# Kernel optimization log

Measured on AMD Instinct MI355X. Metric: run time of the kernel, lower is better.

## Reference

```python
import jax, jax.numpy as jnp
import numpy as np

B, N, K, D_IN, D, L = 8, 8192, 6, 3, 256, 5
EPS_LN = 1e-5


def layernorm(x, g, b):
    m = jnp.mean(x, axis=-1, keepdims=True)
    v = jnp.mean((x - m) ** 2, axis=-1, keepdims=True)
    return (x - m) * jax.lax.rsqrt(v + EPS_LN) * g + b


def spmm_mean(v, knn):
    # sparse adj matmul: out[j] = sum_{n: j in knn[n]} v[n], then / k
    n, k = knn.shape[-2], knn.shape[-1]
    src = jnp.repeat(jnp.arange(n), k)  # [N*K]

    def one(vb, kb):
        return jnp.zeros_like(vb).at[kb.reshape(-1)].add(vb[src])

    return jax.vmap(one)(v, knn) / (k + 1e-6)


def grf_layer(h, knn, qkv_w, out_w, out_b, hops=3):
    q, k, v = jnp.split(h @ qkv_w, 3, axis=-1)
    for _ in range(hops):
        v = spmm_mean(v, knn)
        k = spmm_mean(k, knn)
    attn = jnp.sum(q * k, axis=-1, keepdims=True)
    return (attn * v) @ out_w + out_b


def linear_attention(h, qkv_w, out_w, out_b):
    q, k, v = jnp.split(h @ qkv_w, 3, axis=-1)
    q = jax.nn.relu(q) + 1e-6
    k = jax.nn.relu(k) + 1e-6
    kv = jnp.einsum('bnd,bne->bde', k, v)
    z = 1.0 / (jnp.einsum('bnd,bd->bn', q, k.sum(axis=1)) + 1e-6)
    attn = jnp.einsum('bnd,bde,bn->bne', q, kv, z)
    return attn @ out_w + out_b


def setup_inputs() -> dict:
    key = jax.random.key(0)
    ks = jax.random.split(key, 12)
    s = 0.02
    return {
        'x': jax.random.normal(ks[0], (B, N, D_IN), jnp.float32),
        'knn': jax.random.randint(ks[1], (B, N, K), 0, N, jnp.int32),
        'emb_w': jax.random.normal(ks[2], (D_IN, D), jnp.float32) * s,
        'emb_b': jnp.zeros((D,), jnp.float32),
        'norm_g': jnp.ones((2 * L, D), jnp.float32),
        'norm_b': jnp.zeros((2 * L, D), jnp.float32),
        'grf_qkv': jax.random.normal(ks[3], (L, D, 3 * D), jnp.float32) * s,
        'grf_outw': jax.random.normal(ks[4], (L, D, D), jnp.float32) * s,
        'grf_outb': jnp.zeros((L, D), jnp.float32),
        'attn_qkv': jax.random.normal(ks[5], (L, D, 3 * D), jnp.float32) * s,
        'attn_outw': jax.random.normal(ks[6], (L, D, D), jnp.float32) * s,
        'attn_outb': jnp.zeros((L, D), jnp.float32),
        'head_w': jax.random.normal(ks[7], (D, 3), jnp.float32) * s,
        'head_b': jnp.zeros((3,), jnp.float32),
    }


def reference(x, knn, emb_w, emb_b, norm_g, norm_b, grf_qkv, grf_outw, grf_outb,
              attn_qkv, attn_outw, attn_outb, head_w, head_b):
    h = x @ emb_w + emb_b
    for i in range(L):
        h = h + grf_layer(layernorm(h, norm_g[2 * i], norm_b[2 * i]), knn,
                          grf_qkv[i], grf_outw[i], grf_outb[i])
        h = h + linear_attention(layernorm(h, norm_g[2 * i + 1], norm_b[2 * i + 1]),
                                 attn_qkv[i], attn_outw[i], attn_outb[i])
    return h @ head_w + head_b
```

## Files before the change

kernel.cpp:

```cpp
#include <hip/hip_runtime.h>

#define BB 8
#define NN 8192
#define KK 6
#define DD 256
#define LL 5
#define NE (BB*NN*KK)
#define PLANE (NN*DD)
#define INV6 (1.0f/6.000001f)

typedef unsigned short u16;
typedef __attribute__((ext_vector_type(8))) _Float16 h8;
typedef __attribute__((ext_vector_type(8))) unsigned short us8;
typedef __attribute__((ext_vector_type(4))) float f32x4;

__device__ __forceinline__ u16 f2h(float f){
  union { _Float16 h; u16 u; } c; c.h = (_Float16)f; return c.u;
}
__device__ __forceinline__ float h2f(u16 u){
  union { _Float16 h; u16 u; } c; c.u = u; return (float)c.h;
}

__device__ __forceinline__ void ldscp(const u16* g, u16* l){
  __builtin_amdgcn_global_load_lds(
      (const __attribute__((address_space(1))) void*)g,
      (__attribute__((address_space(3))) void*)l, 16, 0, 0);
}

__global__ void k_count(const int* __restrict__ knn, int* __restrict__ off){
  int e = blockIdx.x*256 + threadIdx.x;
  if(e >= NE) return;
  int b = e / (NN*KK);
  int j = knn[e];
  atomicAdd(&off[b*(NN+1) + 1 + j], 1);
}

__global__ __launch_bounds__(1024) void k_scan(int* __restrict__ offAll){
  __shared__ int lds[1024];
  __shared__ int carry_s;
  int* off = offAll + blockIdx.x*(NN+1);
  const int len = NN+1;
  int t = threadIdx.x;
  if(t==0) carry_s = 0;
  __syncthreads();
  for(int base=0; base<len; base+=1024){
    int x = (base+t < len) ? off[base+t] : 0;
    lds[t] = x; __syncthreads();
    for(int s=1; s<1024; s<<=1){
      int v = (t>=s) ? lds[t-s] : 0;
      __syncthreads();
      lds[t] += v;
      __syncthreads();
    }
    int incl = lds[t];
    int carry = carry_s;
    __syncthreads();
    if(base+t < len) off[base+t] = incl + carry;
    if(t==1023) carry_s = carry + incl;
    __syncthreads();
  }
}

__global__ void k_fill(const int* __restrict__ knn, int* __restrict__ cursor, int* __restrict__ srcE){
  int e = blockIdx.x*256 + threadIdx.x;
  if(e >= NE) return;
  int b = e / (NN*KK);
  int n = (e % (NN*KK)) / KK;
  int j = knn[e];
  int pos = atomicAdd(&cursor[b*(NN+1) + j], 1);
  srcE[(long)b*NN*KK + pos] = n;
}

__global__ __launch_bounds__(256) void k_prepw(const float* __restrict__ W, u16* __restrict__ Wt, int N){
  int n = blockIdx.x, l = blockIdx.y, k = threadIdx.x;
  float x = W[((long)l*256 + k)*N + n];
  u16 hb = f2h(x);
  Wt[(((long)l*2 + 0)*N + n)*256 + k] = hb;
  Wt[(((long)l*2 + 1)*N + n)*256 + k] = f2h(x - h2f(hb));
}

__global__ __launch_bounds__(256) void k_embed(const float* __restrict__ x, const float* __restrict__ ew,
                        const float* __restrict__ eb, float* __restrict__ h){
  int g = blockIdx.x, z = blockIdx.y, d = threadIdx.x;
  const float* xp = x + ((long)z*NN + g)*3;
  h[(long)z*PLANE + (long)g*DD + d] = xp[0]*ew[0*DD+d] + xp[1]*ew[1*DD+d] + xp[2]*ew[2*DD+d] + eb[d];
}

__global__ __launch_bounds__(256) void k_ln(const float* __restrict__ h, const float* __restrict__ g,
                     const float* __restrict__ bia, u16* __restrict__ out){
  long z = blockIdx.y;
  int row = blockIdx.x*4 + (threadIdx.x >> 6);
  int lane = threadIdx.x & 63;
  const float4 x = *(const float4*)(h + z*PLANE + (long)row*DD + lane*4);
  float s  = x.x + x.y + x.z + x.w;
  float s2 = x.x*x.x + x.y*x.y + x.z*x.z + x.w*x.w;
  for(int o=1;o<64;o<<=1){ s += __shfl_xor(s,o); s2 += __shfl_xor(s2,o); }
  float m = s*(1.0f/256.0f);
  float var = s2*(1.0f/256.0f) - m*m;
  float r = rsqrtf(var + 1e-5f);
  const float4 gu = *(const float4*)(g + lane*4);
  const float4 bu = *(const float4*)(bia + lane*4);
  ushort4 o4;
  o4.x = f2h((x.x-m)*r*gu.x + bu.x);
  o4.y = f2h((x.y-m)*r*gu.y + bu.y);
  o4.z = f2h((x.z-m)*r*gu.z + bu.z);
  o4.w = f2h((x.w-m)*r*gu.w + bu.w);
  *(ushort4*)(out + z*PLANE + (long)row*DD + lane*4) = o4;
}

template<int BM,int BN,bool ASPLIT,bool BF32,bool BSPLIT>
__global__ __launch_bounds__(256) void k_mgemm(
    const u16* __restrict__ A, long aStride, long aLoOff, int K, int kSplit,
    const void* __restrict__ Bv, long bStride, long bLoOff,
    const float* __restrict__ rowscale, long rsStride,
    const float* __restrict__ bias,
    u16* __restrict__ o0, u16* __restrict__ o1, u16* __restrict__ o2,
    long oStride, int reluMask, long oLoOff,
    float* __restrict__ accOut, long hStride)
{
  constexpr int WM = BM/2, WN = BN/2, MT = WM/16, NT = WN/16;
  constexpr int STG = BM*32*(ASPLIT?2:1) + BN*32*(BSPLIT?2:1);
  constexpr int EPI = (BM==128) ? 32*132*2 : 0;
  constexpr int SM  = (STG > EPI) ? STG : EPI;
  __shared__ __align__(16) u16 smem[SM];
  u16* Ahi = smem;
  u16* Alo = smem + BM*32;
  u16* Bhi = smem + BM*32*(ASPLIT?2:1);
  u16* Blo = Bhi + BN*32;
  float* epi = (float*)smem;

  const int t = threadIdx.x;
  const int nz = blockIdx.z;
  const long z = nz / kSplit;
  const int chunk = nz % kSplit;
  const int kLen = K / kSplit, kLo = chunk * kLen;
  const int rowTile = blockIdx.x*BM, colTile = blockIdx.y*BN;
  const int l = t & 63, w = t >> 6;
  const int wr = w >> 1, wc = w & 1;
  const int lm = l & 15, kq = l >> 4;

  f32x4 acc[MT][NT];
  #pragma unroll
  for(int mt=0;mt<MT;mt++)
    #pragma unroll
    for(int nt=0;nt<NT;nt++) acc[mt][nt] = (f32x4){0.f,0.f,0.f,0.f};

  for(int k0=kLo; k0<kLo+kLen; k0+=32){
    __syncthreads();
    {
      constexpr int NCH = BM/64;
      #pragma unroll
      for(int li=0; li<NCH; li++){
        int f = li*256 + t;
        int row = f>>2, c = (f&3)*8;
        const u16* gp = A + z*aStride + (long)(rowTile+row)*K + k0 + c;
        ldscp(gp, &Ahi[f*8]);
        if constexpr (ASPLIT) ldscp(gp + aLoOff, &Alo[f*8]);
      }
    }
    if constexpr (BF32){
      constexpr int NCH = BN/64;
      #pragma unroll
      for(int li=0; li<NCH; li++){
        int f = li*256 + t;
        int row = f>>2, c = (f&3)*8;
        const float* src = (const float*)Bv + z*bStride + (long)(colTile+row)*K + k0 + c;
        float4 v0 = ((const float4*)src)[0], v1 = ((const float4*)src)[1];
        us8 hv;
        hv[0]=f2h(v0.x); hv[1]=f2h(v0.y); hv[2]=f2h(v0.z); hv[3]=f2h(v0.w);
        hv[4]=f2h(v1.x); hv[5]=f2h(v1.y); hv[6]=f2h(v1.z); hv[7]=f2h(v1.w);
        *(us8*)&Bhi[f*8] = hv;
      }
    } else {
      constexpr int NCH = BN/64;
      #pragma unroll
      for(int li=0; li<NCH; li++){
        int f = li*256 + t;
        int row = f>>2, c = (f&3)*8;
        const u16* gp = (const u16*)Bv + z*bStride + (long)(colTile+row)*K + k0 + c;
        ldscp(gp, &Bhi[f*8]);
        if constexpr (BSPLIT) ldscp(gp + bLoOff, &Blo[f*8]);
      }
    }
    __syncthreads();
    h8 ah[MT], al[MT], bh[NT], bl[NT];
    #pragma unroll
    for(int mt=0;mt<MT;mt++){
      int idx = (wr*WM + mt*16 + lm)*32 + kq*8;
      ah[mt] = *(const h8*)&Ahi[idx];
      if constexpr (ASPLIT) al[mt] = *(const h8*)&Alo[idx];
    }
    #pragma unroll
    for(int nt=0;nt<NT;nt++){
      int idx = (wc*WN + nt*16 + lm)*32 + kq*8;
      bh[nt] = *(const h8*)&Bhi[idx];
      if constexpr (BSPLIT) bl[nt] = *(const h8*)&Blo[idx];
    }
    #pragma unroll
    for(int mt=0;mt<MT;mt++)
      #pragma unroll
      for(int nt=0;nt<NT;nt++){
        acc[mt][nt] = __builtin_amdgcn_mfma_f32_16x16x32_f16(ah[mt], bh[nt], acc[mt][nt], 0, 0, 0);
        if constexpr (BSPLIT)
          acc[mt][nt] = __builtin_amdgcn_mfma_f32_16x16x32_f16(ah[mt], bl[nt], acc[mt][nt], 0, 0, 0);
        if constexpr (ASPLIT)
          acc[mt][nt] = __builtin_amdgcn_mfma_f32_16x16x32_f16(al[mt], bh[nt], acc[mt][nt], 0, 0, 0);
      }
  }

  if constexpr (BM == 128){
    const int sec = colTile >> 8;
    u16* osec = (sec==0) ? o0 : ((sec==1) ? o1 : o2);
    const bool relu = (reluMask >> sec) & 1;
    #pragma unroll
    for(int mt=0;mt<MT;mt++){
      __syncthreads();
      #pragma unroll
      for(int r=0;r<4;r++){
        int gm = rowTile + wr*64 + mt*16 + kq*4 + r;
        float sc = rowscale ? rowscale[z*rsStride + gm] : 1.0f;
        int rl = wr*16 + kq*4 + r;
        #pragma unroll
        for(int nt=0;nt<NT;nt++)
          epi[rl*132 + wc*64 + nt*16 + lm] = acc[mt][nt][r]*sc;
      }
      __syncthreads();
      #pragma unroll
      for(int ss=0;ss<2;ss++){
        int s = ss*256 + t;
        int rl = s >> 4, sc8 = (s & 15)*8;
        int gm2 = rowTile + (rl>>4)*64 + mt*16 + (rl & 15);
        float v[8];
        #pragma unroll
        for(int j=0;j<8;j++) v[j] = epi[rl*132 + sc8 + j];
        if(bias){
          const float* bp = bias + colTile + sc8;
          #pragma unroll
          for(int j=0;j<8;j++) v[j] += bp[j];
        }
        if(accOut){
          float* hp = accOut + z*hStride + (long)gm2*256 + colTile + sc8;
          float4 h0 = ((float4*)hp)[0], h1 = ((float4*)hp)[1];
          h0.x += v[0]; h0.y += v[1]; h0.z += v[2]; h0.w += v[3];
          h1.x += v[4]; h1.y += v[5]; h1.z += v[6]; h1.w += v[7];
          ((float4*)hp)[0] = h0; ((float4*)hp)[1] = h1;
        } else {
          us8 o8;
          #pragma unroll
          for(int j=0;j<8;j++){
            float vv = v[j];
            if(relu) vv = fmaxf(vv, 0.f) + 1e-6f;
            o8[j] = f2h(vv);
          }
          *(us8*)(osec + z*oStride + (long)gm2*256 + ((colTile + sc8) & 255)) = o8;
        }
      }
    }
  } else {
    #pragma unroll
    for(int mt=0;mt<MT;mt++){
      #pragma unroll
      for(int r=0;r<4;r++){
        int gm = rowTile + wr*WM + mt*16 + kq*4 + r;
        float sc = rowscale ? rowscale[z*rsStride + gm] : 1.0f;
        if(accOut){
          float* hp = accOut + z*hStride + (long)gm*256;
          if(kSplit > 1){
            #pragma unroll
            for(int nt=0;nt<NT;nt++){
              int gc = colTile + wc*WN + nt*16 + lm;
              atomicAdd(&hp[gc], acc[mt][nt][r]);
            }
          } else {
            #pragma unroll
            for(int nt=0;nt<NT;nt++){
              int gc = colTile + wc*WN + nt*16 + lm;
              hp[gc] += acc[mt][nt][r]*sc + (bias ? bias[gc] : 0.f);
            }
          }
        } else {
          #pragma unroll
          for(int nt=0;nt<NT;nt++){
            int gc = colTile + wc*WN + nt*16 + lm;
            int sec = gc >> 8;
            u16* o = (sec==0) ? o0 : ((sec==1) ? o1 : o2);
            float val = acc[mt][nt][r]*sc + (bias ? bias[gc] : 0.f);
            if((reluMask >> sec) & 1) val = fmaxf(val, 0.f) + 1e-6f;
            if(sec==0 && oLoOff){
              u16* oo = o0 + 2*z*oStride + (long)gm*256 + (gc & 255);
              u16 hb = f2h(val);
              oo[0] = hb;
              oo[oLoOff] = f2h(val - h2f(hb));
            } else {
              o[z*oStride + (long)gm*256 + (gc & 255)] = f2h(val);
            }
          }
        }
      }
    }
  }
}

__global__ __launch_bounds__(256) void k_fusedout(
    const u16* __restrict__ A, const u16* __restrict__ B, long bStride, long bLoOff,
    const float* __restrict__ rowscale, const float* __restrict__ bias,
    float* __restrict__ h,
    const float* __restrict__ lnG, const float* __restrict__ lnB,
    u16* __restrict__ Lout)
{
  constexpr int SMU = 64*32 + 2*256*32;
  __shared__ __align__(16) u16 smem[SMU];
  u16* As = smem;
  u16* Bh = smem + 64*32;
  u16* Bl = Bh + 256*32;
  float* epi = (float*)smem;

  const int t = threadIdx.x;
  const long z = blockIdx.z;
  const int rowTile = blockIdx.x*64;
  const int l = t & 63, w = t >> 6;
  const int wr = w >> 1, wc = w & 1;
  const int lm = l & 15, kq = l >> 4;
  const u16* Ab = A + z*PLANE;
  const u16* Bb = B + z*bStride;

  f32x4 acc[2][8];
  #pragma unroll
  for(int mt=0;mt<2;mt++)
    #pragma unroll
    for(int nt=0;nt<8;nt++) acc[mt][nt] = (f32x4){0.f,0.f,0.f,0.f};

  for(int k0=0; k0<256; k0+=32){
    __syncthreads();
    {
      ldscp(Ab + (long)(rowTile+(t>>2))*256 + k0 + (t&3)*8, &As[t*8]);
    }
    #pragma unroll
    for(int li=0; li<4; li++){
      int f = li*256 + t;
      int row = f>>2, c = (f&3)*8;
      const u16* gp = Bb + (long)row*256 + k0 + c;
      ldscp(gp, &Bh[f*8]);
      ldscp(gp + bLoOff, &Bl[f*8]);
    }
    __syncthreads();
    h8 af[2], bh[8], bl[8];
    #pragma unroll
    for(int mt=0;mt<2;mt++)
      af[mt] = *(const h8*)&As[(wr*32 + mt*16 + lm)*32 + kq*8];
    #pragma unroll
    for(int nt=0;nt<8;nt++){
      int idx = (wc*128 + nt*16 + lm)*32 + kq*8;
      bh[nt] = *(const h8*)&Bh[idx];
      bl[nt] = *(const h8*)&Bl[idx];
    }
    #pragma unroll
    for(int mt=0;mt<2;mt++)
      #pragma unroll
      for(int nt=0;nt<8;nt++){
        acc[mt][nt] = __builtin_amdgcn_mfma_f32_16x16x32_f16(af[mt], bh[nt], acc[mt][nt], 0, 0, 0);
        acc[mt][nt] = __builtin_amdgcn_mfma_f32_16x16x32_f16(af[mt], bl[nt], acc[mt][nt], 0, 0, 0);
      }
  }

  #pragma unroll
  for(int mt=0;mt<2;mt++){
    __syncthreads();
    #pragma unroll
    for(int r=0;r<4;r++){
      int rl = wr*16 + kq*4 + r;
      int gm = rowTile + wr*32 + mt*16 + kq*4 + r;
      float sc = rowscale ? rowscale[z*NN + gm] : 1.0f;
      #pragma unroll
      for(int nt=0;nt<8;nt++)
        epi[rl*260 + wc*128 + nt*16 + lm] = acc[mt][nt][r]*sc;
    }
    __syncthreads();
    #pragma unroll
    for(int ss=0;ss<8;ss++){
      int s = ss*256 + t;
      int rl = s >> 6;
      int c4 = (s & 63)*4;
      int gm = rowTile + (rl>>4)*32 + mt*16 + (rl & 15);
      float4 e = *(float4*)&epi[rl*260 + c4];
      float4 x;
      x.x = e.x + bias[c4+0];
      x.y = e.y + bias[c4+1];
      x.z = e.z + bias[c4+2];
      x.w = e.w + bias[c4+3];
      float* hp = h + z*PLANE + (long)gm*256 + c4;
      float4 h0 = *(float4*)hp;
      x.x += h0.x; x.y += h0.y; x.z += h0.z; x.w += h0.w;
      *(float4*)hp = x;
      if(lnG){
        float sA = x.x + x.y + x.z + x.w;
        float s2 = x.x*x.x + x.y*x.y + x.z*x.z + x.w*x.w;
        for(int o=1;o<64;o<<=1){ sA += __shfl_xor(sA,o); s2 += __shfl_xor(s2,o); }
        float m = sA*(1.0f/256.0f);
        float var = s2*(1.0f/256.0f) - m*m;
        float rr = rsqrtf(var + 1e-5f);
        const float4 gu = *(const float4*)(lnG + c4);
        const float4 bu = *(const float4*)(lnB + c4);
        ushort4 o4;
        o4.x = f2h((x.x-m)*rr*gu.x + bu.x);
        o4.y = f2h((x.y-m)*rr*gu.y + bu.y);
        o4.z = f2h((x.z-m)*rr*gu.z + bu.z);
        o4.w = f2h((x.w-m)*rr*gu.w + bu.w);
        *(ushort4*)(Lout + z*PLANE + (long)gm*256 + c4) = o4;
      }
    }
  }
}

template<int MODE>
__global__ __launch_bounds__(256) void k_spmm2(
    const u16* __restrict__ kin, const u16* __restrict__ vin,
    const int* __restrict__ offB, const int* __restrict__ srcB,
    u16* __restrict__ kout, u16* __restrict__ vout,
    const u16* __restrict__ q, float* __restrict__ rs){
  long z = blockIdx.x;
  const int* off = offB + z*(NN+1);
  const int* sE  = srcB + z*(long)NN*KK;

  if constexpr (MODE == 0){
    const u16* kp = kin + z*PLANE;
    const u16* vp = vin + z*PLANE;
    int row = blockIdx.y*16 + (threadIdx.x >> 4);
    int d8 = blockIdx.z*128 + (threadIdx.x & 15)*8;
    int s0 = off[row], s1 = off[row+1];
    float ak[8], av[8];
    #pragma unroll
    for(int j=0;j<8;j++){ ak[j]=0.f; av[j]=0.f; }
    int e = s0;
    for(; e+1 < s1; e += 2){
      int n0 = sE[e], n1 = sE[e+1];
      us8 k0 = *(const us8*)(kp + (long)n0*DD + d8);
      us8 k1 = *(const us8*)(kp + (long)n1*DD + d8);
      us8 v0 = *(const us8*)(vp + (long)n0*DD + d8);
      us8 v1 = *(const us8*)(vp + (long)n1*DD + d8);
      #pragma unroll
      for(int j=0;j<8;j++){
        ak[j] += h2f(k0[j]) + h2f(k1[j]);
        av[j] += h2f(v0[j]) + h2f(v1[j]);
      }
    }
    if(e < s1){
      int n0 = sE[e];
      us8 k0 = *(const us8*)(kp + (long)n0*DD + d8);
      us8 v0 = *(const us8*)(vp + (long)n0*DD + d8);
      #pragma unroll
      for(int j=0;j<8;j++){ ak[j] += h2f(k0[j]); av[j] += h2f(v0[j]); }
    }
    us8 ok, ov;
    #pragma unroll
    for(int j=0;j<8;j++){ ok[j] = f2h(ak[j]*INV6); ov[j] = f2h(av[j]*INV6); }
    *(us8*)(kout + z*PLANE + (long)row*DD + d8) = ok;
    *(us8*)(vout + z*PLANE + (long)row*DD + d8) = ov;
  } else {
    if(blockIdx.z == 0){
      const u16* kp = kin + z*PLANE;
      int row = blockIdx.y*8 + (threadIdx.x >> 5);
      int l32 = threadIdx.x & 31;
      int d8 = l32*8;
      int s0 = off[row], s1 = off[row+1];
      float ak[8];
      #pragma unroll
      for(int j=0;j<8;j++) ak[j]=0.f;
      int e = s0;
      for(; e+1 < s1; e += 2){
        int n0 = sE[e], n1 = sE[e+1];
        us8 k0 = *(const us8*)(kp + (long)n0*DD + d8);
        us8 k1 = *(const us8*)(kp + (long)n1*DD + d8);
        #pragma unroll
        for(int j=0;j<8;j++) ak[j] += h2f(k0[j]) + h2f(k1[j]);
      }
      if(e < s1){
        int n0 = sE[e];
        us8 k0 = *(const us8*)(kp + (long)n0*DD + d8);
        #pragma unroll
        for(int j=0;j<8;j++) ak[j] += h2f(k0[j]);
      }
      us8 qv = *(const us8*)(q + z*PLANE + (long)row*DD + d8);
      float s = 0.f;
      #pragma unroll
      for(int j=0;j<8;j++) s += h2f(qv[j]) * ak[j];
      for(int o=1;o<32;o<<=1) s += __shfl_xor(s,o);
      if(l32==0) rs[z*NN + row] = s*INV6;
    } else {
      const u16* vp = vin + z*PLANE;
      int row = (blockIdx.y & 511)*16 + (threadIdx.x >> 4);
      int d8 = (blockIdx.y >> 9)*128 + (threadIdx.x & 15)*8;
      int s0 = off[row], s1 = off[row+1];
      float av[8];
      #pragma unroll
      for(int j=0;j<8;j++) av[j]=0.f;
      int e = s0;
      for(; e+1 < s1; e += 2){
        int n0 = sE[e], n1 = sE[e+1];
        us8 v0 = *(const us8*)(vp + (long)n0*DD + d8);
        us8 v1 = *(const us8*)(vp + (long)n1*DD + d8);
        #pragma unroll
        for(int j=0;j<8;j++) av[j] += h2f(v0[j]) + h2f(v1[j]);
      }
      if(e < s1){
        int n0 = sE[e];
        us8 v0 = *(const us8*)(vp + (long)n0*DD + d8);
        #pragma unroll
        for(int j=0;j<8;j++) av[j] += h2f(v0[j]);
      }
      us8 ov;
      #pragma unroll
      for(int j=0;j<8;j++) ov[j] = f2h(av[j]*INV6);
      *(us8*)(vout + z*PLANE + (long)row*DD + d8) = ov;
    }
  }
}

__global__ __launch_bounds__(256) void k_zcalc(const u16* __restrict__ q, const float* __restrict__ ksum,
                        float* __restrict__ rs){
  long z = blockIdx.y;
  int row = blockIdx.x*4 + (threadIdx.x >> 6);
  int lane = threadIdx.x & 63;
  ushort4 qv = *(const ushort4*)(q + z*PLANE + (long)row*DD + lane*4);
  const float4 c = *(const float4*)(ksum + z*DD + lane*4);
  float s = h2f(qv.x)*c.x + h2f(qv.y)*c.y + h2f(qv.z)*c.z + h2f(qv.w)*c.w;
  for(int o=1;o<64;o<<=1) s += __shfl_xor(s,o);
  if(lane==0) rs[z*NN + row] = 1.0f / (s + 1e-6f);
}

__global__ __launch_bounds__(256) void k_transp2(
    const u16* __restrict__ in0, u16* __restrict__ out0,
    const u16* __restrict__ in1, u16* __restrict__ out1){
  __shared__ u16 tile[64][72];
  int zz = blockIdx.z;
  long z = zz >> 1;
  const u16* ip = ((zz & 1) ? in1 : in0) + z*PLANE;
  u16* op = ((zz & 1) ? out1 : out0) + z*PLANE;
  int r0 = blockIdx.x*64, c0 = blockIdx.y*64;
  int t = threadIdx.x;
  {
    int r = t>>2, cg = (t&3)*16;
    *(us8*)&tile[r][cg]   = *(const us8*)(ip + (long)(r0+r)*DD + c0 + cg);
    *(us8*)&tile[r][cg+8] = *(const us8*)(ip + (long)(r0+r)*DD + c0 + cg + 8);
  }
  __syncthreads();
  {
    int c = t>>2, rg = t&3;
    us8 a, b;
    #pragma unroll
    for(int j=0;j<8;j++){ a[j] = tile[rg*16+j][c]; b[j] = tile[rg*16+8+j][c]; }
    u16* dst = op + (long)(c0+c)*NN + r0 + rg*16;
    *(us8*)dst = a; *(us8*)(dst+8) = b;
  }
}

__global__ __launch_bounds__(256) void k_ksum(const u16* __restrict__ kT, float* __restrict__ ksum){
  long z = blockIdx.y;
  int d = blockIdx.x;
  const u16* p = kT + z*PLANE + (long)d*NN;
  float s = 0.f;
  for(int i=threadIdx.x*8; i<NN; i+=2048){
    us8 a = *(const us8*)(p+i);
    #pragma unroll
    for(int j=0;j<8;j++) s += h2f(a[j]);
  }
  for(int o=1;o<64;o<<=1) s += __shfl_xor(s,o);
  __shared__ float ws4[4];
  int w = threadIdx.x >> 6;
  if((threadIdx.x & 63)==0) ws4[w] = s;
  __syncthreads();
  if(threadIdx.x==0) ksum[z*DD + d] = ws4[0]+ws4[1]+ws4[2]+ws4[3];
}

__global__ __launch_bounds__(256) void k_head(const float* __restrict__ h, const float* __restrict__ hw,
                       const float* __restrict__ hb, float* __restrict__ out){
  long z = blockIdx.y;
  int row = blockIdx.x*4 + (threadIdx.x >> 6);
  int lane = threadIdx.x & 63;
  const float4 x = *(const float4*)(h + z*PLANE + (long)row*DD + lane*4);
  int d0 = lane*4;
  float a0 = x.x*hw[(d0+0)*3+0] + x.y*hw[(d0+1)*3+0] + x.z*hw[(d0+2)*3+0] + x.w*hw[(d0+3)*3+0];
  float a1 = x.x*hw[(d0+0)*3+1] + x.y*hw[(d0+1)*3+1] + x.z*hw[(d0+2)*3+1] + x.w*hw[(d0+3)*3+1];
  float a2 = x.x*hw[(d0+0)*3+2] + x.y*hw[(d0+1)*3+2] + x.z*hw[(d0+2)*3+2] + x.w*hw[(d0+3)*3+2];
  for(int o=1;o<64;o<<=1){
    a0 += __shfl_xor(a0,o); a1 += __shfl_xor(a1,o); a2 += __shfl_xor(a2,o);
  }
  if(lane==0){
    float* op = out + (z*NN + row)*3;
    op[0] = a0 + hb[0];
    op[1] = a1 + hb[1];
    op[2] = a2 + hb[2];
  }
}

struct Carve {
  float *h; u16 *L,*Q,*Bp,*Cp,*T;
  float *kvf; u16 *w2t;
  float *ksum,*rs;
  int *off,*cursor,*srcE;
  u16 *wt_gqkv,*wt_aqkv,*wt_gout,*wt_aout;
  size_t total;
};

static Carve carve(char* base, int C){
  Carve c;
  size_t cur = 0;
  auto bump = [&](size_t bytes)->char*{
    char* p = base ? base + cur : (char*)0;
    cur += (bytes + 255) & ~(size_t)255;
    return p;
  };
  c.h    = (float*)bump((size_t)C*PLANE*4);
  c.L    = (u16*)bump((size_t)C*PLANE*2);
  c.Q    = (u16*)bump((size_t)C*PLANE*2);
  c.Bp   = (u16*)bump((size_t)C*PLANE*2);
  c.Cp   = (u16*)bump((size_t)C*PLANE*2);
  c.T    = (u16*)bump((size_t)C*PLANE*2);
  c.kvf  = (float*)bump((size_t)C*DD*DD*4);
  c.w2t  = (u16*)bump((size_t)C*2*DD*DD*2);
  c.ksum = (float*)bump((size_t)C*DD*4);
  c.rs   = (float*)bump((size_t)C*NN*4);
  c.off  = (int*)bump((size_t)BB*(NN+1)*4);
  c.cursor=(int*)bump((size_t)BB*(NN+1)*4);
  c.srcE = (int*)bump((size_t)NE*4);
  c.wt_gqkv = (u16*)bump((size_t)LL*2*768*256*2);
  c.wt_aqkv = (u16*)bump((size_t)LL*2*768*256*2);
  c.wt_gout = (u16*)bump((size_t)LL*2*256*256*2);
  c.wt_aout = (u16*)bump((size_t)LL*2*256*256*2);
  c.total = cur;
  return c;
}

extern "C" void kernel_launch(void* const* d_in, const int* in_sizes, int n_in,
                              void* d_out, int out_size, void* d_ws, size_t ws_size,
                              hipStream_t stream)
{
  const float* x        = (const float*)d_in[0];
  const int*   knn      = (const int*)d_in[1];
  const float* emb_w    = (const float*)d_in[2];
  const float* emb_b    = (const float*)d_in[3];
  const float* norm_g   = (const float*)d_in[4];
  const float* norm_b   = (const float*)d_in[5];
  const float* grf_qkv  = (const float*)d_in[6];
  const float* grf_outw = (const float*)d_in[7];
  const float* grf_outb = (const float*)d_in[8];
  const float* attn_qkv = (const float*)d_in[9];
  const float* attn_outw= (const float*)d_in[10];
  const float* attn_outb= (const float*)d_in[11];
  const float* head_w   = (const float*)d_in[12];
  const float* head_b   = (const float*)d_in[13];
  float* out = (float*)d_out;

  int C = 1;
  for(int cc=BB; cc>=1; cc>>=1){ if(carve(nullptr, cc).total <= ws_size){ C = cc; break; } }
  Carve ws = carve((char*)d_ws, C);

  k_prepw<<<dim3(768, LL), 256, 0, stream>>>(grf_qkv,  ws.wt_gqkv, 768);
  k_prepw<<<dim3(768, LL), 256, 0, stream>>>(attn_qkv, ws.wt_aqkv, 768);
  k_prepw<<<dim3(256, LL), 256, 0, stream>>>(grf_outw, ws.wt_gout, 256);
  k_prepw<<<dim3(256, LL), 256, 0, stream>>>(attn_outw,ws.wt_aout, 256);

  hipMemsetAsync(ws.off, 0, (size_t)BB*(NN+1)*sizeof(int), stream);
  k_count<<<dim3((NE+255)/256), 256, 0, stream>>>(knn, ws.off);
  k_scan<<<dim3(BB), 1024, 0, stream>>>(ws.off);
  hipMemcpyAsync(ws.cursor, ws.off, (size_t)BB*(NN+1)*sizeof(int), hipMemcpyDeviceToDevice, stream);
  k_fill<<<dim3((NE+255)/256), 256, 0, stream>>>(knn, ws.cursor, ws.srcE);

  const long PL = PLANE;
  for(int b0=0; b0<BB; b0+=C){
    const int* offB  = ws.off  + (long)b0*(NN+1);
    const int* srcB  = ws.srcE + (long)b0*NN*KK;

    k_embed<<<dim3(NN, C), 256, 0, stream>>>(x + (long)b0*NN*3, emb_w, emb_b, ws.h);
    k_ln<<<dim3(NN/4, C), 256, 0, stream>>>(ws.h, norm_g, norm_b, ws.L);

    for(int i=0; i<LL; i++){
      k_mgemm<128,128,false,false,true><<<dim3(64, 6, C), 256, 0, stream>>>(
          ws.L, PL, 0, 256, 1,
          ws.wt_gqkv + (long)i*2*768*256, 0, (long)768*256,
          nullptr, 0, nullptr,
          ws.Q, ws.Bp, ws.Cp, PL, 0, 0, nullptr, 0);
      k_spmm2<0><<<dim3(C, NN/16, 2), 256, 0, stream>>>(ws.Bp, ws.Cp, offB, srcB, ws.L, ws.T, nullptr, nullptr);
      k_spmm2<0><<<dim3(C, NN/16, 2), 256, 0, stream>>>(ws.L,  ws.T,  offB, srcB, ws.Bp, ws.Cp, nullptr, nullptr);
      k_spmm2<1><<<dim3(C, NN/8, 2), 256, 0, stream>>>(ws.Bp, ws.Cp, offB, srcB, nullptr, ws.T, ws.Q, ws.rs);
      k_fusedout<<<dim3(NN/64, 1, C), 256, 0, stream>>>(
          ws.T, ws.wt_gout + (long)i*2*256*256, 0, (long)256*256,
          ws.rs, grf_outb + (long)i*DD, ws.h,
          norm_g + (2*i+1)*DD, norm_b + (2*i+1)*DD, ws.L);

      k_mgemm<128,128,false,false,true><<<dim3(64, 6, C), 256, 0, stream>>>(
          ws.L, PL, 0, 256, 1,
          ws.wt_aqkv + (long)i*2*768*256, 0, (long)768*256,
          nullptr, 0, nullptr,
          ws.Q, ws.Bp, ws.Cp, PL, 3 , 0, nullptr, 0);
      k_transp2<<<dim3(NN/64, DD/64, 2*C), 256, 0, stream>>>(ws.Bp, ws.L, ws.Cp, ws.T);
      k_ksum<<<dim3(DD, C), 256, 0, stream>>>(ws.L, ws.ksum);
      hipMemsetAsync(ws.kvf, 0, (size_t)C*DD*DD*sizeof(float), stream);
      k_mgemm<64,64,false,false,false><<<dim3(4, 4, C*8), 256, 0, stream>>>(
          ws.L, PL, 0, NN, 8,
          ws.T, PL, 0,
          nullptr, 0, nullptr,
          nullptr, nullptr, nullptr, 0, 0, 0, ws.kvf, (long)DD*DD);
      k_mgemm<64,64,true,true,false><<<dim3(4, 4, C), 256, 0, stream>>>(
          ws.wt_aout + (long)i*2*256*256, 0, (long)256*256, 256, 1,
          ws.kvf, (long)DD*DD, 0,
          nullptr, 0, nullptr,
          ws.w2t, nullptr, nullptr, (long)DD*DD, 0, (long)DD*DD,
          nullptr, 0);
      k_zcalc<<<dim3(NN/4, C), 256, 0, stream>>>(ws.Q, ws.ksum, ws.rs);
      const float* g2 = (i==LL-1) ? nullptr : norm_g + (2*i+2)*DD;
      const float* b2 = (i==LL-1) ? nullptr : norm_b + (2*i+2)*DD;
      k_fusedout<<<dim3(NN/64, 1, C), 256, 0, stream>>>(
          ws.Q, ws.w2t, 2L*DD*DD, (long)DD*DD,
          ws.rs, attn_outb + (long)i*DD, ws.h,
          g2, b2, ws.L);
    }

    k_head<<<dim3(NN/4, C), 256, 0, stream>>>(ws.h, head_w, head_b, out + (long)b0*NN*3);
  }
}
```

Measured before the change: 2.550 ms.

## Halve fusedout row tile and keep A fragments in registers

The fused output GEMM now uses 32-row tiles instead of 64 and launches twice as many blocks. Each wave loads its whole A row-fragment set straight into registers, so only B goes through LDS. The hi and lo B planes are streamed in two separate passes through one smaller LDS buffer. The aim is higher occupancy and more blocks for a small GEMM, at the cost of more B reloads per output row and more barriers per block.

```diff
diff --git a/kernel.cpp b/kernel.cpp
--- a/kernel.cpp
+++ b/kernel.cpp
@@ -308,80 +308,72 @@
     const float* __restrict__ lnG, const float* __restrict__ lnB,
     u16* __restrict__ Lout)
 {
-  constexpr int SMU = 64*32 + 2*256*32;
-  __shared__ __align__(16) u16 smem[SMU];
-  u16* As = smem;
-  u16* Bh = smem + 64*32;
-  u16* Bl = Bh + 256*32;
+  __shared__ __align__(16) u16 smem[8320];
+  u16* Bs = smem;
   float* epi = (float*)smem;
 
   const int t = threadIdx.x;
   const long z = blockIdx.z;
-  const int rowTile = blockIdx.x*64;
+  const int rowTile = blockIdx.x*32;
   const int l = t & 63, w = t >> 6;
   const int wr = w >> 1, wc = w & 1;
   const int lm = l & 15, kq = l >> 4;
   const u16* Ab = A + z*PLANE;
   const u16* Bb = B + z*bStride;
 
-  f32x4 acc[2][8];
+  f32x4 acc[8];
   #pragma unroll
-  for(int mt=0;mt<2;mt++)
-    #pragma unroll
-    for(int nt=0;nt<8;nt++) acc[mt][nt] = (f32x4){0.f,0.f,0.f,0.f};
-
-  for(int k0=0; k0<256; k0+=32){
+  for(int nt=0;nt<8;nt++) acc[nt] = (f32x4){0.f,0.f,0.f,0.f};
+
+  h8 areg[8];
+  {
+    const u16* arow = Ab + (long)(rowTile + wr*16 + lm)*256 + kq*8;
+    #pragma unroll
+    for(int kk=0;kk<8;kk++) areg[kk] = *(const h8*)(arow + kk*32);
+  }
+
+  #pragma unroll
+  for(int pass=0; pass<2; ++pass){
+    const u16* Bp = Bb + (pass ? bLoOff : 0);
+    #pragma unroll
+    for(int kk=0; kk<8; ++kk){
+      __syncthreads();
+      #pragma unroll
+      for(int li=0; li<4; li++){
+        int f = li*256 + t;
+        int row = f>>2, c = (f&3)*8;
+        ldscp(Bp + (long)row*256 + kk*32 + c, &Bs[f*8]);
+      }
+      __syncthreads();
+      #pragma unroll
+      for(int nt=0;nt<8;nt++){
+        const h8 bf = *(const h8*)&Bs[(wc*128 + nt*16 + lm)*32 + kq*8];
+        acc[nt] = __builtin_amdgcn_mfma_f32_16x16x32_f16(areg[kk], bf, acc[nt], 0, 0, 0);
+      }
+    }
+  }
+
+  #pragma unroll
+  for(int p=0;p<2;p++){
     __syncthreads();
-    {
-      ldscp(Ab + (long)(rowTile+(t>>2))*256 + k0 + (t&3)*8, &As[t*8]);
-    }
-    #pragma unroll
-    for(int li=0; li<4; li++){
-      int f = li*256 + t;
-      int row = f>>2, c = (f&3)*8;
-      const u16* gp = Bb + (long)row*256 + k0 + c;
-      ldscp(gp, &Bh[f*8]);
-      ldscp(gp + bLoOff, &Bl[f*8]);
+    if(wr == p){
+      #pragma unroll
+      for(int r=0;r<4;r++){
+        int rl = kq*4 + r;
+        int gm = rowTile + p*16 + rl;
+        float sc = rowscale ? rowscale[z*NN + gm] : 1.0f;
+        #pragma unroll
+        for(int nt=0;nt<8;nt++)
+          epi[rl*260 + wc*128 + nt*16 + lm] = acc[nt][r]*sc;
+      }
     }
     __syncthreads();
-    h8 af[2], bh[8], bl[8];
-    #pragma unroll
-    for(int mt=0;mt<2;mt++)
-      af[mt] = *(const h8*)&As[(wr*32 + mt*16 + lm)*32 + kq*8];
-    #pragma unroll
-    for(int nt=0;nt<8;nt++){
-      int idx = (wc*128 + nt*16 + lm)*32 + kq*8;
-      bh[nt] = *(const h8*)&Bh[idx];
-      bl[nt] = *(const h8*)&Bl[idx];
-    }
-    #pragma unroll
-    for(int mt=0;mt<2;mt++)
-      #pragma unroll
-      for(int nt=0;nt<8;nt++){
-        acc[mt][nt] = __builtin_amdgcn_mfma_f32_16x16x32_f16(af[mt], bh[nt], acc[mt][nt], 0, 0, 0);
-        acc[mt][nt] = __builtin_amdgcn_mfma_f32_16x16x32_f16(af[mt], bl[nt], acc[mt][nt], 0, 0, 0);
-      }
-  }
-
-  #pragma unroll
-  for(int mt=0;mt<2;mt++){
-    __syncthreads();
-    #pragma unroll
-    for(int r=0;r<4;r++){
-      int rl = wr*16 + kq*4 + r;
-      int gm = rowTile + wr*32 + mt*16 + kq*4 + r;
-      float sc = rowscale ? rowscale[z*NN + gm] : 1.0f;
-      #pragma unroll
-      for(int nt=0;nt<8;nt++)
-        epi[rl*260 + wc*128 + nt*16 + lm] = acc[mt][nt][r]*sc;
-    }
-    __syncthreads();
-    #pragma unroll
-    for(int ss=0;ss<8;ss++){
+    #pragma unroll
+    for(int ss=0;ss<4;ss++){
       int s = ss*256 + t;
       int rl = s >> 6;
       int c4 = (s & 63)*4;
-      int gm = rowTile + (rl>>4)*32 + mt*16 + (rl & 15);
+      int gm = rowTile + p*16 + rl;
       float4 e = *(float4*)&epi[rl*260 + c4];
       float4 x;
       x.x = e.x + bias[c4+0];
@@ -683,7 +675,7 @@
       k_spmm2<0><<<dim3(C, NN/16, 2), 256, 0, stream>>>(ws.Bp, ws.Cp, offB, srcB, ws.L, ws.T, nullptr, nullptr);
       k_spmm2<0><<<dim3(C, NN/16, 2), 256, 0, stream>>>(ws.L,  ws.T,  offB, srcB, ws.Bp, ws.Cp, nullptr, nullptr);
       k_spmm2<1><<<dim3(C, NN/8, 2), 256, 0, stream>>>(ws.Bp, ws.Cp, offB, srcB, nullptr, ws.T, ws.Q, ws.rs);
-      k_fusedout<<<dim3(NN/64, 1, C), 256, 0, stream>>>(
+      k_fusedout<<<dim3(NN/32, 1, C), 256, 0, stream>>>(
           ws.T, ws.wt_gout + (long)i*2*256*256, 0, (long)256*256,
           ws.rs, grf_outb + (long)i*DD, ws.h,
           norm_g + (2*i+1)*DD, norm_b + (2*i+1)*DD, ws.L);
@@ -710,7 +702,7 @@
       k_zcalc<<<dim3(NN/4, C), 256, 0, stream>>>(ws.Q, ws.ksum, ws.rs);
       const float* g2 = (i==LL-1) ? nullptr : norm_g + (2*i+2)*DD;
       const float* b2 = (i==LL-1) ? nullptr : norm_b + (2*i+2)*DD;
-      k_fusedout<<<dim3(NN/64, 1, C), 256, 0, stream>>>(
+      k_fusedout<<<dim3(NN/32, 1, C), 256, 0, stream>>>(
           ws.Q, ws.w2t, 2L*DD*DD, (long)DD*DD,
           ws.rs, attn_outb + (long)i*DD, ws.h,
           g2, b2, ws.L);
```

New measurement: 2.543 ms. No clear change (-0.3%).
